# Performance work log

Hardware: AMD Instinct MI355X
Metric: run time of the kernel (lower is better)

Reference implementation:

```python
import jax, jax.numpy as jnp
import numpy as np

N_NODES = 50000
N_EDGES = 800000
F_IN = 24
H = 128
N_GRAPHS = 100
BN_EPS = 1e-5


def setup_inputs() -> dict:
    key = jax.random.key(0)
    ks = jax.random.split(key, 12)
    x = jax.random.normal(ks[0], (N_NODES, F_IN), dtype=jnp.float32)
    edge_index = jax.random.randint(ks[1], (2, N_EDGES), 0, N_NODES, dtype=jnp.int32)
    batch = (jnp.arange(N_NODES, dtype=jnp.int32) // (N_NODES // N_GRAPHS)).astype(jnp.int32)

    def lin(k, fan_in, fan_out):
        bound = 1.0 / np.sqrt(fan_in)
        kw, kb = jax.random.split(k)
        W = jax.random.uniform(kw, (fan_in, fan_out), jnp.float32, -bound, bound)
        b = jax.random.uniform(kb, (fan_out,), jnp.float32, -bound, bound)
        return W, b

    W1, b1 = lin(ks[2], 2 * F_IN, H)
    W2, b2 = lin(ks[3], 2 * H, H)
    W3, b3 = lin(ks[4], 2 * H, H)
    Wl, bl = lin(ks[5], H, 1)
    g1 = jnp.ones((H,), jnp.float32); be1 = jnp.zeros((H,), jnp.float32)
    g2 = jnp.ones((H,), jnp.float32); be2 = jnp.zeros((H,), jnp.float32)
    g3 = jnp.ones((H,), jnp.float32); be3 = jnp.zeros((H,), jnp.float32)
    return {"x": x, "edge_index": edge_index, "batch": batch,
            "W1": W1, "b1": b1, "W2": W2, "b2": b2, "W3": W3, "b3": b3,
            "g1": g1, "be1": be1, "g2": g2, "be2": be2, "g3": g3, "be3": be3,
            "Wl": Wl, "bl": bl}


def edge_conv(x, src, dst, W, b):
    # PyG EdgeConv: message = mlp([x_i, x_j - x_i]) for edge j->i, aggr=max at i
    x_i = x[dst]                                    # [E, F]
    e = jnp.concatenate([x_i, x[src] - x_i], axis=-1)  # [E, 2F]
    m = jax.nn.relu(e @ W + b)                      # [E, H]
    out = jax.ops.segment_max(m, dst, num_segments=N_NODES)
    return jnp.where(jnp.isfinite(out), out, 0.0)   # isolated nodes -> 0


def batch_norm(h, g, b):
    # training-mode BN over node dim (biased variance), dropout treated as identity
    mu = h.mean(axis=0)
    var = ((h - mu) ** 2).mean(axis=0)
    return g * (h - mu) * jax.lax.rsqrt(var + BN_EPS) + b


def reference(x, edge_index, batch, W1, b1, W2, b2, W3, b3,
              g1, be1, g2, be2, g3, be3, Wl, bl):
    src, dst = edge_index[0], edge_index[1]
    h = edge_conv(x, src, dst, W1, b1)
    h = jax.nn.relu(batch_norm(h, g1, be1))
    h = edge_conv(h, src, dst, W2, b2)
    h = jax.nn.relu(batch_norm(h, g2, be2))
    h = edge_conv(h, src, dst, W3, b3)
    h = batch_norm(h, g3, be3)
    # global_mean_pool
    sums = jax.ops.segment_sum(h, batch, num_segments=N_GRAPHS)           # [G, H]
    counts = jax.ops.segment_sum(jnp.ones((h.shape[0],), h.dtype), batch,
                                 num_segments=N_GRAPHS)
    pooled = sums / jnp.maximum(counts, 1.0)[:, None]
    return jax.nn.relu(pooled @ Wl + bl)                                  # [G, 1]
```

## Files before the change

kernel.cpp:

```cpp
#include <hip/hip_runtime.h>

#define N_NODES 50000
#define N_EDGES 800000
#define F_IN 24
#define HDIM 128
#define N_GRAPHS 100
#define BN_EPS 1e-5f
#define NBLK 196
#define ROWS_PER_GRAPH (N_NODES / N_GRAPHS)
#define MM_GRID 782
#define HIST_BLKS ((N_EDGES + 255) / 256)
#define PREP_BLKS (F_IN + 2 * HDIM)
#define SSTR 32
#define SUMS_PER_LAYER (256 * SSTR)
#define STATS_BLKS 392
#define POOL_CHUNKS 10
#define POOL_BLKS (N_GRAPHS * POOL_CHUNKS)
#define ROWS_PER_CHUNK (ROWS_PER_GRAPH / POOL_CHUNKS)


typedef _Float16 h2 __attribute__((ext_vector_type(2)));
typedef _Float16 h4 __attribute__((ext_vector_type(4)));
typedef _Float16 f16x8 __attribute__((ext_vector_type(8)));
typedef float f32x4 __attribute__((ext_vector_type(4)));

template <int K, int KC>
__global__ __launch_bounds__(256) void k_mm1(const float* __restrict__ X,
                                             const float* __restrict__ Wcat,
                                             const float* __restrict__ bias,
                                             float* __restrict__ A, _Float16* __restrict__ C) {
    __shared__ float Xs[KC * 68];
    __shared__ float Ws[KC * 256];
    int tid = threadIdx.x;
    int row0 = blockIdx.x * 64;
    int cg = tid & 31;
    int rg = tid >> 5;

    float accA[8][4], accC[8][4];
#pragma unroll
    for (int ri = 0; ri < 8; ++ri)
#pragma unroll
        for (int ci = 0; ci < 4; ++ci) {
            accA[ri][ci] = bias[cg * 4 + ci];
            accC[ri][ci] = 0.f;
        }

    for (int k0 = 0; k0 < K; k0 += KC) {
        __syncthreads();
        {
            const int C4 = KC / 4;
            for (int i = tid; i < 64 * C4; i += 256) {
                int c4 = i % C4, r = i / C4;
                int row = row0 + r;
                float4 v = make_float4(0.f, 0.f, 0.f, 0.f);
                if (row < N_NODES) v = *(const float4*)&X[row * K + k0 + c4 * 4];
                Xs[(c4 * 4 + 0) * 68 + r] = v.x;
                Xs[(c4 * 4 + 1) * 68 + r] = v.y;
                Xs[(c4 * 4 + 2) * 68 + r] = v.z;
                Xs[(c4 * 4 + 3) * 68 + r] = v.w;
            }
        }
        for (int i = tid; i < KC * 64; i += 256) {
            int c4 = i & 63, kr = i >> 6;
            *(float4*)&Ws[kr * 256 + c4 * 4] =
                *(const float4*)&Wcat[(k0 + kr) * 256 + c4 * 4];
        }
        __syncthreads();
#pragma unroll
        for (int kk = 0; kk < KC; ++kk) {
            float4 t0 = *(const float4*)&Xs[kk * 68 + rg * 8];
            float4 t1 = *(const float4*)&Xs[kk * 68 + rg * 8 + 4];
            float4 wa = *(const float4*)&Ws[kk * 256 + cg * 4];
            float4 wc = *(const float4*)&Ws[kk * 256 + 128 + cg * 4];
            float t[8] = {t0.x, t0.y, t0.z, t0.w, t1.x, t1.y, t1.z, t1.w};
            float wav[4] = {wa.x, wa.y, wa.z, wa.w};
            float wcv[4] = {wc.x, wc.y, wc.z, wc.w};
#pragma unroll
            for (int ri = 0; ri < 8; ++ri)
#pragma unroll
                for (int ci = 0; ci < 4; ++ci) {
                    accA[ri][ci] += t[ri] * wav[ci];
                    accC[ri][ci] += t[ri] * wcv[ci];
                }
        }
    }

#pragma unroll
    for (int ri = 0; ri < 8; ++ri) {
        int row = row0 + rg * 8 + ri;
        if (row < N_NODES) {
            *(float4*)&A[row * HDIM + cg * 4] =
                make_float4(accA[ri][0], accA[ri][1], accA[ri][2], accA[ri][3]);
            union { h2 h[2]; uint2 u; } pk;
            pk.h[0] = h2{(_Float16)accC[ri][0], (_Float16)accC[ri][1]};
            pk.h[1] = h2{(_Float16)accC[ri][2], (_Float16)accC[ri][3]};
            *(uint2*)&C[row * HDIM + cg * 4] = pk.u;
        }
    }
}

__global__ __launch_bounds__(256) void k_mmf(const _Float16* __restrict__ X,
                                             const _Float16* __restrict__ Wf,
                                             const float* __restrict__ bias,
                                             const float* __restrict__ sums,
                                             const float* __restrict__ g,
                                             const float* __restrict__ be,
                                             float* __restrict__ A, _Float16* __restrict__ C) {
    __shared__ _Float16 Xh[16 * 520];
    __shared__ _Float16 Wh[128 * 128];
    __shared__ float scs[128], shs[128];
    int tid = threadIdx.x;
    int lane = tid & 63, wv = tid >> 6;
    int row0 = blockIdx.x * 64;

    if (tid < 128) {
        float S  = sums[tid * SSTR];
        float S2 = sums[(128 + tid) * SSTR];
        float mean = S / (float)N_NODES;
        float var = fmaxf(S2 / (float)N_NODES - mean * mean, 0.f);
        float scv = g[tid] / sqrtf(var + BN_EPS);
        scs[tid] = scv;
        shs[tid] = be[tid] - mean * scv;
    }
    {
        const uint4* s = (const uint4*)Wf;
        uint4* d = (uint4*)Wh;
        for (int i = tid; i < 2048; i += 256) d[i] = s[i];
    }
    __syncthreads();
    for (int i = tid; i < 64 * 32; i += 256) {
        int k4 = i & 31, rl = i >> 5;
        int row = row0 + rl;
        float4 v = make_float4(0.f, 0.f, 0.f, 0.f);
        if (row < N_NODES) {
            h4 xv = *(const h4*)&X[row * HDIM + k4 * 4];
            v = make_float4((float)xv.x, (float)xv.y, (float)xv.z, (float)xv.w);
        }
        int c = k4 * 4;
        v.x = fmaxf(v.x * scs[c + 0] + shs[c + 0], 0.f);
        v.y = fmaxf(v.y * scs[c + 1] + shs[c + 1], 0.f);
        v.z = fmaxf(v.z * scs[c + 2] + shs[c + 2], 0.f);
        v.w = fmaxf(v.w * scs[c + 3] + shs[c + 3], 0.f);
        int rt = rl >> 4, m = rl & 15, kc = k4 >> 3, q = (k4 >> 1) & 3, jh = k4 & 1;
        _Float16* dp = Xh + (rt * 4 + kc) * 520 + (q * 16 + m) * 8 + jh * 4;
        dp[0] = (_Float16)v.x; dp[1] = (_Float16)v.y;
        dp[2] = (_Float16)v.z; dp[3] = (_Float16)v.w;
    }
    __syncthreads();

    int n = lane & 15, q = lane >> 4;
    f32x4 acc[8];

#pragma unroll
    for (int nt = 0; nt < 8; ++nt) {
        float b0 = bias[nt * 16 + n];
        acc[nt] = f32x4{b0, b0, b0, b0};
    }
#pragma unroll
    for (int kc = 0; kc < 4; ++kc) {
        f16x8 a = *(const f16x8*)(Xh + (wv * 4 + kc) * 520 + lane * 8);
#pragma unroll
        for (int nt = 0; nt < 8; ++nt) {
            f16x8 b = *(const f16x8*)(Wh + ((nt * 4 + kc) * 64 + lane) * 8);
            acc[nt] = __builtin_amdgcn_mfma_f32_16x16x32_f16(a, b, acc[nt], 0, 0, 0);
        }
    }
#pragma unroll
    for (int nt = 0; nt < 8; ++nt) {
#pragma unroll
        for (int r = 0; r < 4; ++r) {
            int row = row0 + wv * 16 + q * 4 + r;
            if (row < N_NODES) A[row * HDIM + nt * 16 + n] = acc[nt][r];
        }
    }
    __syncthreads();
    {
        const uint4* s = (const uint4*)(Wf + 16384);
        uint4* d = (uint4*)Wh;
        for (int i = tid; i < 2048; i += 256) d[i] = s[i];
    }
    __syncthreads();

#pragma unroll
    for (int nt = 0; nt < 8; ++nt) acc[nt] = f32x4{0.f, 0.f, 0.f, 0.f};
#pragma unroll
    for (int kc = 0; kc < 4; ++kc) {
        f16x8 a = *(const f16x8*)(Xh + (wv * 4 + kc) * 520 + lane * 8);
#pragma unroll
        for (int nt = 0; nt < 8; ++nt) {
            f16x8 b = *(const f16x8*)(Wh + ((nt * 4 + kc) * 64 + lane) * 8);
            acc[nt] = __builtin_amdgcn_mfma_f32_16x16x32_f16(a, b, acc[nt], 0, 0, 0);
        }
    }
#pragma unroll
    for (int nt = 0; nt < 8; ++nt) {
#pragma unroll
        for (int r = 0; r < 4; ++r) {
            int row = row0 + wv * 16 + q * 4 + r;
            if (row < N_NODES) C[row * HDIM + nt * 16 + n] = (_Float16)acc[nt][r];
        }
    }
}

__global__ void k_pre(const float* __restrict__ W1, const float* __restrict__ W2,
                      const float* __restrict__ W3, float* __restrict__ Wcat1,
                      _Float16* __restrict__ Wf2, _Float16* __restrict__ Wf3,
                      const int* __restrict__ dst, unsigned* __restrict__ deg,
                      unsigned* __restrict__ rank) {
    int b = blockIdx.x;
    int j = threadIdx.x;
    if (b < F_IN) {
        float wb = W1[(b + F_IN) * HDIM + (j & 127)];
        float wt = W1[b * HDIM + (j & 127)];
        Wcat1[b * 256 + j] = (j < HDIM) ? (wt - wb) : wb;
    } else if (b < PREP_BLKS) {
        int idx = b - F_IN;
        int layer = idx >> 7;
        int k = idx & 127;
        const float* W = layer ? W3 : W2;
        _Float16* Wf   = layer ? Wf3 : Wf2;
        int col = j & 127;
        float wt = W[k * HDIM + col];
        float wb = W[(k + HDIM) * HDIM + col];
        float v = (j < 128) ? (wt - wb) : wb;
        int plane = j >> 7;
        int nt = col >> 4, n = col & 15, kc = k >> 5, q = (k >> 3) & 3, jj = k & 7;
        int f = ((nt * 4 + kc) * 4 + q) * 128 + n * 8 + jj;
        Wf[plane * 16384 + f] = (_Float16)v;
    } else {
        int e = (b - PREP_BLKS) * 256 + j;
        if (e < N_EDGES) rank[e] = atomicAdd(&deg[dst[e]], 1u);
    }
}

__global__ __launch_bounds__(256) void k_scanall(const unsigned* __restrict__ deg,
                                                 unsigned* __restrict__ bsum,
                                                 unsigned* __restrict__ off) {
    __shared__ unsigned s[256];
    int t = threadIdx.x;
    int b = blockIdx.x;
    int i = b * 256 + t;
    unsigned v = (i < N_NODES) ? deg[i] : 0u;
    s[t] = v;
    __syncthreads();
    for (int d = 1; d < 256; d <<= 1) {
        unsigned u = (t >= d) ? s[t - d] : 0u;
        __syncthreads();
        s[t] += u;
        __syncthreads();
    }
    unsigned locex = s[t] - v;
    if (t == 255) atomicExch(&bsum[b], s[255] + 1u);
    __syncthreads();
    unsigned bs = 0;
    if (t < NBLK) {
        unsigned x;
        do { x = atomicAdd(&bsum[t], 0u); } while (x == 0u);
        bs = x - 1u;
    }
    s[t] = (t < NBLK) ? bs : 0u;
    __syncthreads();
    for (int d = 1; d < 256; d <<= 1) {
        unsigned u = (t >= d) ? s[t - d] : 0u;
        __syncthreads();
        s[t] += u;
        __syncthreads();
    }
    unsigned bexcl = (b == 0) ? 0u : s[b - 1];
    if (i < N_NODES) off[i] = bexcl + locex;
}

__global__ void k_scatter(const int* __restrict__ src, const int* __restrict__ dst,
                          const unsigned* __restrict__ off, const unsigned* __restrict__ rank,
                          unsigned* __restrict__ ssrc) {
    int e = blockIdx.x * 256 + threadIdx.x;
    if (e < N_EDGES)
        ssrc[off[dst[e]] + rank[e]] = (unsigned)src[e];
}

__global__ __launch_bounds__(256) void k_agg(const float* __restrict__ A,
                                             const h2* __restrict__ Cc,
                                             const unsigned* __restrict__ off,
                                             const unsigned* __restrict__ deg,
                                             const unsigned* __restrict__ ssrc,
                                             h2* __restrict__ H) {
    __shared__ unsigned sl[4][64];
    int w = threadIdx.x >> 6;
    int lane = threadIdx.x & 63;
    int i = blockIdx.x * 4 + w;
    int d = (int)deg[i];
    unsigned o = off[i];
    float2 a = *(const float2*)&A[i * HDIM + lane * 2];
    union { unsigned short us[2]; h2 v; } ninf;
    ninf.us[0] = 0xFC00; ninf.us[1] = 0xFC00;
    const h2 NI = ninf.v;
    h2 m2 = NI;
    for (int base = 0; base < d; base += 64) {
        int cntc = min(64, d - base);
        if (lane < cntc) sl[w][lane] = ssrc[o + base + lane];
        int e = 0;
        for (; e + 16 <= cntc; e += 16) {
            unsigned s[16];
#pragma unroll
            for (int j = 0; j < 16; ++j) s[j] = sl[w][e + j];
            h2 v[16];
#pragma unroll
            for (int j = 0; j < 16; ++j) v[j] = Cc[s[j] * 64 + lane];
#pragma unroll
            for (int st = 8; st > 0; st >>= 1)
#pragma unroll
                for (int j = 0; j < st; ++j)
                    v[j] = __builtin_elementwise_max(v[j], v[j + st]);
            m2 = __builtin_elementwise_max(m2, v[0]);
        }
        if (e + 8 <= cntc) {
            unsigned s[8];
#pragma unroll
            for (int j = 0; j < 8; ++j) s[j] = sl[w][e + j];
            h2 v[8];
#pragma unroll
            for (int j = 0; j < 8; ++j) v[j] = Cc[s[j] * 64 + lane];
#pragma unroll
            for (int st = 4; st > 0; st >>= 1)
#pragma unroll
                for (int j = 0; j < st; ++j)
                    v[j] = __builtin_elementwise_max(v[j], v[j + st]);
            m2 = __builtin_elementwise_max(m2, v[0]);
            e += 8;
        }
        if (e < cntc) {
            int last = cntc - 1;
            unsigned s[8];
#pragma unroll
            for (int j = 0; j < 8; ++j) {
                int idx = e + j;
                s[j] = sl[w][idx < last ? idx : last];
            }
            h2 v[8];
#pragma unroll
            for (int j = 0; j < 8; ++j) v[j] = Cc[s[j] * 64 + lane];
#pragma unroll
            for (int j = 0; j < 8; ++j)
                if (e + j >= cntc) v[j] = NI;
#pragma unroll
            for (int st = 4; st > 0; st >>= 1)
#pragma unroll
                for (int j = 0; j < st; ++j)
                    v[j] = __builtin_elementwise_max(v[j], v[j + st]);
            m2 = __builtin_elementwise_max(m2, v[0]);
        }
    }
    float hx = (d > 0) ? fmaxf(a.x + (float)m2.x, 0.f) : 0.f;
    float hy = (d > 0) ? fmaxf(a.y + (float)m2.y, 0.f) : 0.f;
    H[i * 64 + lane] = h2{(_Float16)hx, (_Float16)hy};
}

__global__ __launch_bounds__(256) void k_stats(const _Float16* __restrict__ H,
                                               float* __restrict__ sums) {
    __shared__ float4 ls[256], ls2[256];
    int t = threadIdx.x;
    int c4 = t & 31, rg = t >> 5;
    int row0 = blockIdx.x * 128;
    float4 s = make_float4(0.f, 0.f, 0.f, 0.f);
    float4 s2 = make_float4(0.f, 0.f, 0.f, 0.f);
#pragma unroll 4
    for (int it = 0; it < 16; ++it) {
        int row = row0 + rg * 16 + it;
        if (row < N_NODES) {
            h4 hv = *(const h4*)&H[row * HDIM + c4 * 4];
            float4 v = make_float4((float)hv.x, (float)hv.y, (float)hv.z, (float)hv.w);
            s.x += v.x; s.y += v.y; s.z += v.z; s.w += v.w;
            s2.x += v.x * v.x; s2.y += v.y * v.y; s2.z += v.z * v.z; s2.w += v.w * v.w;
        }
    }
    ls[t] = s; ls2[t] = s2;
    __syncthreads();
    if (t < 32) {
        float4 a = ls[t], a2 = ls2[t];
#pragma unroll
        for (int j = 1; j < 8; ++j) {
            float4 b = ls[j * 32 + t], b2 = ls2[j * 32 + t];
            a.x += b.x; a.y += b.y; a.z += b.z; a.w += b.w;
            a2.x += b2.x; a2.y += b2.y; a2.z += b2.z; a2.w += b2.w;
        }
        int c = t * 4;
        atomicAdd(&sums[(c + 0) * SSTR], a.x);
        atomicAdd(&sums[(c + 1) * SSTR], a.y);
        atomicAdd(&sums[(c + 2) * SSTR], a.z);
        atomicAdd(&sums[(c + 3) * SSTR], a.w);
        atomicAdd(&sums[(128 + c + 0) * SSTR], a2.x);
        atomicAdd(&sums[(128 + c + 1) * SSTR], a2.y);
        atomicAdd(&sums[(128 + c + 2) * SSTR], a2.z);
        atomicAdd(&sums[(128 + c + 3) * SSTR], a2.w);
    }
}

__global__ __launch_bounds__(256) void k_pool2(const _Float16* __restrict__ H,
                                               float* __restrict__ Pp,
                                               float* __restrict__ sums) {
    __shared__ float4 ls[256], ls2[256];
    int t = threadIdx.x;
    int c4 = t & 31, rg = t >> 5;
    int b = blockIdx.x;
    int base = (b / POOL_CHUNKS) * ROWS_PER_GRAPH + (b % POOL_CHUNKS) * ROWS_PER_CHUNK;
    float4 s = make_float4(0.f, 0.f, 0.f, 0.f);
    float4 s2 = make_float4(0.f, 0.f, 0.f, 0.f);
#pragma unroll
    for (int j = 0; j < 7; ++j) {
        int rl = rg + j * 8;
        if (rl < ROWS_PER_CHUNK) {
            int row = base + rl;
            h4 hv = *(const h4*)&H[row * HDIM + c4 * 4];
            float4 v = make_float4((float)hv.x, (float)hv.y, (float)hv.z, (float)hv.w);
            s.x += v.x; s.y += v.y; s.z += v.z; s.w += v.w;
            s2.x += v.x * v.x; s2.y += v.y * v.y; s2.z += v.z * v.z; s2.w += v.w * v.w;
        }
    }
    ls[t] = s; ls2[t] = s2;
    __syncthreads();
    if (t < 32) {
        float4 a = ls[t], a2 = ls2[t];
#pragma unroll
        for (int j = 1; j < 8; ++j) {
            float4 q = ls[j * 32 + t], q2 = ls2[j * 32 + t];
            a.x += q.x; a.y += q.y; a.z += q.z; a.w += q.w;
            a2.x += q2.x; a2.y += q2.y; a2.z += q2.z; a2.w += q2.w;
        }
        int c = t * 4;
        *(float4*)&Pp[b * HDIM + c] = a;
        atomicAdd(&sums[(c + 0) * SSTR], a.x);
        atomicAdd(&sums[(c + 1) * SSTR], a.y);
        atomicAdd(&sums[(c + 2) * SSTR], a.z);
        atomicAdd(&sums[(c + 3) * SSTR], a.w);
        atomicAdd(&sums[(128 + c + 0) * SSTR], a2.x);
        atomicAdd(&sums[(128 + c + 1) * SSTR], a2.y);
        atomicAdd(&sums[(128 + c + 2) * SSTR], a2.z);
        atomicAdd(&sums[(128 + c + 3) * SSTR], a2.w);
    }
}

__global__ __launch_bounds__(128) void k_out(const float* __restrict__ Pp,
                                             const float* __restrict__ sums,
                                             const float* __restrict__ g3,
                                             const float* __restrict__ be3,
                                             const float* __restrict__ Wl,
                                             const float* __restrict__ bl,
                                             float* __restrict__ out) {
    int g = blockIdx.x;
    int k = threadIdx.x;
    float S  = sums[k * SSTR];
    float S2 = sums[(128 + k) * SSTR];
    float mean = S / (float)N_NODES;
    float var = fmaxf(S2 / (float)N_NODES - mean * mean, 0.f);
    float scv = g3[k] / sqrtf(var + BN_EPS);
    float shv = be3[k] - mean * scv;
    float pooled = 0.f;
#pragma unroll
    for (int j = 0; j < POOL_CHUNKS; ++j)
        pooled += Pp[(g * POOL_CHUNKS + j) * HDIM + k];
    float p = (scv * (pooled * (1.f / (float)ROWS_PER_GRAPH)) + shv) * Wl[k];
    __shared__ float red[2];
    for (int o = 32; o > 0; o >>= 1) p += __shfl_down(p, o);
    if ((k & 63) == 0) red[k >> 6] = p;
    __syncthreads();
    if (k == 0) out[g] = fmaxf(red[0] + red[1] + bl[0], 0.f);
}

extern "C" void kernel_launch(void* const* d_in, const int* in_sizes, int n_in,
                              void* d_out, int out_size, void* d_ws, size_t ws_size,
                              hipStream_t stream) {
    const float* x   = (const float*)d_in[0];
    const int* ei    = (const int*)d_in[1];
    const float* W1  = (const float*)d_in[3];
    const float* b1  = (const float*)d_in[4];
    const float* W2  = (const float*)d_in[5];
    const float* b2  = (const float*)d_in[6];
    const float* W3  = (const float*)d_in[7];
    const float* b3  = (const float*)d_in[8];
    const float* g1  = (const float*)d_in[9];
    const float* be1 = (const float*)d_in[10];
    const float* g2  = (const float*)d_in[11];
    const float* be2 = (const float*)d_in[12];
    const float* g3  = (const float*)d_in[13];
    const float* be3 = (const float*)d_in[14];
    const float* Wl  = (const float*)d_in[15];
    const float* bl  = (const float*)d_in[16];
    float* out = (float*)d_out;

    const int* srcp = ei;
    const int* dstp = ei + N_EDGES;

    char* ws = (char*)d_ws;
    size_t o = 0;
    auto alloc = [&](size_t bytes) -> void* {
        o = (o + 255) & ~(size_t)255;
        void* p = ws + o;
        o += bytes;
        return p;
    };
    float* A      = (float*)alloc((size_t)N_NODES * HDIM * 4);
    _Float16* C   = (_Float16*)alloc((size_t)N_NODES * HDIM * 2);
    _Float16* h   = (_Float16*)alloc((size_t)N_NODES * HDIM * 2);
    float* Wcat1  = (float*)alloc((size_t)F_IN * 256 * 4);
    _Float16* Wf2 = (_Float16*)alloc((size_t)2 * 16384 * 2);
    _Float16* Wf3 = (_Float16*)alloc((size_t)2 * 16384 * 2);
    unsigned* deg  = (unsigned*)alloc((size_t)N_NODES * 4);
    unsigned* bsum = (unsigned*)alloc((size_t)NBLK * 4);
    float* sums    = (float*)alloc((size_t)3 * SUMS_PER_LAYER * 4);
    unsigned* off  = (unsigned*)alloc((size_t)N_NODES * 4);
    unsigned* rank = (unsigned*)alloc((size_t)N_EDGES * 4);
    unsigned* ssrc = (unsigned*)alloc((size_t)N_EDGES * 4);
    float* Pp      = (float*)alloc((size_t)POOL_BLKS * HDIM * 4);
    (void)ws_size; (void)n_in; (void)in_sizes; (void)out_size;

    float* sums0 = sums;
    float* sums1 = sums + SUMS_PER_LAYER;
    float* sums2 = sums + 2 * SUMS_PER_LAYER;

    size_t zlen = (size_t)((char*)(sums + 3 * SUMS_PER_LAYER) - (char*)deg);
    (void)hipMemsetAsync(deg, 0, zlen, stream);

    k_pre<<<PREP_BLKS + HIST_BLKS, 256, 0, stream>>>(W1, W2, W3, Wcat1, Wf2, Wf3,
                                                     dstp, deg, rank);
    k_scanall<<<NBLK, 256, 0, stream>>>(deg, bsum, off);
    k_scatter<<<HIST_BLKS, 256, 0, stream>>>(srcp, dstp, off, rank, ssrc);

    const int AGB = N_NODES / 4;

    k_mm1<F_IN, F_IN><<<MM_GRID, 256, 0, stream>>>(x, Wcat1, b1, A, C);
    k_agg<<<AGB, 256, 0, stream>>>(A, (const h2*)C, off, deg, ssrc, (h2*)h);
    k_stats<<<STATS_BLKS, 256, 0, stream>>>(h, sums0);

    k_mmf<<<MM_GRID, 256, 0, stream>>>(h, Wf2, b2, sums0, g1, be1, A, C);
    k_agg<<<AGB, 256, 0, stream>>>(A, (const h2*)C, off, deg, ssrc, (h2*)h);
    k_stats<<<STATS_BLKS, 256, 0, stream>>>(h, sums1);

    k_mmf<<<MM_GRID, 256, 0, stream>>>(h, Wf3, b3, sums1, g2, be2, A, C);
    k_agg<<<AGB, 256, 0, stream>>>(A, (const h2*)C, off, deg, ssrc, (h2*)h);

    k_pool2<<<POOL_BLKS, 256, 0, stream>>>(h, Pp, sums2);
    k_out<<<N_GRAPHS, 128, 0, stream>>>(Pp, sums2, g3, be3, Wl, bl, out);
}
```

Baseline: 366.1 us.

## Split aggregation across channel quarters with edge-parallel lanes and shuffled indices

The max-aggregation kernel is restructured so each wavefront handles one 32-channel quarter of a node. Its 64 lanes are split into 4 edge groups of 16 channel lanes, which are combined with xor-shuffles at the end. Neighbor indices are passed between lanes with __shfl instead of staged in LDS. This makes 4x more blocks and more independent gathers per wave. It also re-reads the index list once per quarter and uses 64-byte row segments instead of 256-byte ones, which may hurt coalescing.

```diff
diff --git a/kernel.cpp b/kernel.cpp
--- a/kernel.cpp
+++ b/kernel.cpp
@@ -17,12 +17,21 @@
 #define POOL_CHUNKS 10
 #define POOL_BLKS (N_GRAPHS * POOL_CHUNKS)
 #define ROWS_PER_CHUNK (ROWS_PER_GRAPH / POOL_CHUNKS)
+#define AGB (N_NODES / 4)
+#define AGQ 4
 
 
 typedef _Float16 h2 __attribute__((ext_vector_type(2)));
 typedef _Float16 h4 __attribute__((ext_vector_type(4)));
 typedef _Float16 f16x8 __attribute__((ext_vector_type(8)));
 typedef float f32x4 __attribute__((ext_vector_type(4)));
+
+__device__ inline h2 shfl_xor_h2(h2 v, int mask) {
+    union { h2 h; int i; } u;
+    u.h = v;
+    u.i = __shfl_xor(u.i, mask);
+    return u.h;
+}
 
 template <int K, int KC>
 __global__ __launch_bounds__(256) void k_mm1(const float* __restrict__ X,
@@ -284,75 +293,71 @@
                                              const unsigned* __restrict__ deg,
                                              const unsigned* __restrict__ ssrc,
                                              h2* __restrict__ H) {
-    __shared__ unsigned sl[4][64];
     int w = threadIdx.x >> 6;
     int lane = threadIdx.x & 63;
-    int i = blockIdx.x * 4 + w;
+    int bid = blockIdx.x;
+    int q = bid / AGB;
+    int nb = bid - q * AGB;
+    int i = nb * 4 + w;
     int d = (int)deg[i];
     unsigned o = off[i];
-    float2 a = *(const float2*)&A[i * HDIM + lane * 2];
+    int ch = lane & 15;
+    int es = lane >> 4;
+    const h2* Cq = Cc + q * 16;
+    float2 a = make_float2(0.f, 0.f);
+    if (lane < 16) a = *(const float2*)&A[i * HDIM + q * 32 + lane * 2];
     union { unsigned short us[2]; h2 v; } ninf;
     ninf.us[0] = 0xFC00; ninf.us[1] = 0xFC00;
     const h2 NI = ninf.v;
     h2 m2 = NI;
     for (int base = 0; base < d; base += 64) {
-        int cntc = min(64, d - base);
-        if (lane < cntc) sl[w][lane] = ssrc[o + base + lane];
+        int cnt = min(64, d - base);
+        int idxv = 0;
+        if (lane < cnt) idxv = (int)ssrc[o + base + lane];
         int e = 0;
-        for (; e + 16 <= cntc; e += 16) {
-            unsigned s[16];
-#pragma unroll
-            for (int j = 0; j < 16; ++j) s[j] = sl[w][e + j];
-            h2 v[16];
-#pragma unroll
-            for (int j = 0; j < 16; ++j) v[j] = Cc[s[j] * 64 + lane];
-#pragma unroll
-            for (int st = 8; st > 0; st >>= 1)
-#pragma unroll
-                for (int j = 0; j < st; ++j)
-                    v[j] = __builtin_elementwise_max(v[j], v[j + st]);
-            m2 = __builtin_elementwise_max(m2, v[0]);
-        }
-        if (e + 8 <= cntc) {
-            unsigned s[8];
-#pragma unroll
-            for (int j = 0; j < 8; ++j) s[j] = sl[w][e + j];
-            h2 v[8];
-#pragma unroll
-            for (int j = 0; j < 8; ++j) v[j] = Cc[s[j] * 64 + lane];
-#pragma unroll
-            for (int st = 4; st > 0; st >>= 1)
-#pragma unroll
-                for (int j = 0; j < st; ++j)
-                    v[j] = __builtin_elementwise_max(v[j], v[j + st]);
-            m2 = __builtin_elementwise_max(m2, v[0]);
-            e += 8;
-        }
-        if (e < cntc) {
-            int last = cntc - 1;
-            unsigned s[8];
-#pragma unroll
-            for (int j = 0; j < 8; ++j) {
-                int idx = e + j;
-                s[j] = sl[w][idx < last ? idx : last];
-            }
-            h2 v[8];
-#pragma unroll
-            for (int j = 0; j < 8; ++j) v[j] = Cc[s[j] * 64 + lane];
-#pragma unroll
-            for (int j = 0; j < 8; ++j)
-                if (e + j >= cntc) v[j] = NI;
-#pragma unroll
-            for (int st = 4; st > 0; st >>= 1)
-#pragma unroll
-                for (int j = 0; j < st; ++j)
-                    v[j] = __builtin_elementwise_max(v[j], v[j + st]);
-            m2 = __builtin_elementwise_max(m2, v[0]);
-        }
-    }
-    float hx = (d > 0) ? fmaxf(a.x + (float)m2.x, 0.f) : 0.f;
-    float hy = (d > 0) ? fmaxf(a.y + (float)m2.y, 0.f) : 0.f;
-    H[i * 64 + lane] = h2{(_Float16)hx, (_Float16)hy};
+        for (; e + 16 <= cnt; e += 16) {
+            int s0 = __shfl(idxv, e + es);
+            int s1 = __shfl(idxv, e + 4 + es);
+            int s2 = __shfl(idxv, e + 8 + es);
+            int s3 = __shfl(idxv, e + 12 + es);
+            h2 v0 = Cq[(unsigned)s0 * 64 + ch];
+            h2 v1 = Cq[(unsigned)s1 * 64 + ch];
+            h2 v2 = Cq[(unsigned)s2 * 64 + ch];
+            h2 v3 = Cq[(unsigned)s3 * 64 + ch];
+            h2 a0 = __builtin_elementwise_max(v0, v1);
+            h2 a1 = __builtin_elementwise_max(v2, v3);
+            m2 = __builtin_elementwise_max(m2, __builtin_elementwise_max(a0, a1));
+        }
+        if (e < cnt) {
+            int last = cnt - 1;
+            int j0 = e + es,      k0 = j0 < last ? j0 : last;
+            int j1 = e + 4 + es,  k1 = j1 < last ? j1 : last;
+            int j2 = e + 8 + es,  k2 = j2 < last ? j2 : last;
+            int j3 = e + 12 + es, k3 = j3 < last ? j3 : last;
+            int s0 = __shfl(idxv, k0);
+            int s1 = __shfl(idxv, k1);
+            int s2 = __shfl(idxv, k2);
+            int s3 = __shfl(idxv, k3);
+            h2 v0 = Cq[(unsigned)s0 * 64 + ch];
+            h2 v1 = Cq[(unsigned)s1 * 64 + ch];
+            h2 v2 = Cq[(unsigned)s2 * 64 + ch];
+            h2 v3 = Cq[(unsigned)s3 * 64 + ch];
+            if (j0 >= cnt) v0 = NI;
+            if (j1 >= cnt) v1 = NI;
+            if (j2 >= cnt) v2 = NI;
+            if (j3 >= cnt) v3 = NI;
+            h2 a0 = __builtin_elementwise_max(v0, v1);
+            h2 a1 = __builtin_elementwise_max(v2, v3);
+            m2 = __builtin_elementwise_max(m2, __builtin_elementwise_max(a0, a1));
+        }
+    }
+    m2 = __builtin_elementwise_max(m2, shfl_xor_h2(m2, 16));
+    m2 = __builtin_elementwise_max(m2, shfl_xor_h2(m2, 32));
+    if (lane < 16) {
+        float hx = (d > 0) ? fmaxf(a.x + (float)m2.x, 0.f) : 0.f;
+        float hy = (d > 0) ? fmaxf(a.y + (float)m2.y, 0.f) : 0.f;
+        H[i * 64 + q * 16 + lane] = h2{(_Float16)hx, (_Float16)hy};
+    }
 }
 
 __global__ __launch_bounds__(256) void k_stats(const _Float16* __restrict__ H,
@@ -525,18 +530,16 @@
     k_scanall<<<NBLK, 256, 0, stream>>>(deg, bsum, off);
     k_scatter<<<HIST_BLKS, 256, 0, stream>>>(srcp, dstp, off, rank, ssrc);
 
-    const int AGB = N_NODES / 4;
-
     k_mm1<F_IN, F_IN><<<MM_GRID, 256, 0, stream>>>(x, Wcat1, b1, A, C);
-    k_agg<<<AGB, 256, 0, stream>>>(A, (const h2*)C, off, deg, ssrc, (h2*)h);
+    k_agg<<<AGQ * AGB, 256, 0, stream>>>(A, (const h2*)C, off, deg, ssrc, (h2*)h);
     k_stats<<<STATS_BLKS, 256, 0, stream>>>(h, sums0);
 
     k_mmf<<<MM_GRID, 256, 0, stream>>>(h, Wf2, b2, sums0, g1, be1, A, C);
-    k_agg<<<AGB, 256, 0, stream>>>(A, (const h2*)C, off, deg, ssrc, (h2*)h);
+    k_agg<<<AGQ * AGB, 256, 0, stream>>>(A, (const h2*)C, off, deg, ssrc, (h2*)h);
     k_stats<<<STATS_BLKS, 256, 0, stream>>>(h, sums1);
 
     k_mmf<<<MM_GRID, 256, 0, stream>>>(h, Wf3, b3, sums1, g2, be2, A, C);
-    k_agg<<<AGB, 256, 0, stream>>>(A, (const h2*)C, off, deg, ssrc, (h2*)h);
+    k_agg<<<AGQ * AGB, 256, 0, stream>>>(A, (const h2*)C, off, deg, ssrc, (h2*)h);
 
     k_pool2<<<POOL_BLKS, 256, 0, stream>>>(h, Pp, sums2);
     k_out<<<N_GRAPHS, 128, 0, stream>>>(Pp, sums2, g3, be3, Wl, bl, out);
```

Result: slower. 449.1 us (+22.7%).
